# Kernel tuning notes

Measured on AMD Instinct MI355X. Metric: run time of the kernel, lower is better.

Reference implementation:

```python
import jax, jax.numpy as jnp
import numpy as np

STRIDE = 16
RATIOS = (0.5, 1.0, 2.0)
SCALES = (8, 16, 32)
NMS_THRESH = 0.7
NUM_PRE = 12000
NUM_POST = 2000
MIN_SIZE = 16.0


def _all_anchors(feat_h, feat_w):
    # base anchors centered at (stride/2, stride/2), (y1, x1, y2, x2)
    base = []
    for r in RATIOS:
        for s in SCALES:
            h = STRIDE * s * np.sqrt(r)
            w = STRIDE * s * np.sqrt(1.0 / r)
            c = STRIDE / 2.0
            base.append([c - h / 2.0, c - w / 2.0, c + h / 2.0, c + w / 2.0])
    base = np.asarray(base, np.float32)  # (A, 4)
    ys = np.arange(feat_h, dtype=np.float32) * STRIDE
    xs = np.arange(feat_w, dtype=np.float32) * STRIDE
    shift = np.stack(np.meshgrid(ys, xs, indexing='ij'), axis=-1)  # (H, W, 2) = (y, x)
    shift4 = np.concatenate([shift, shift], axis=-1)  # (H, W, 4)
    anchors = shift4[:, :, None, :] + base[None, None, :, :]  # (H, W, A, 4)
    return jnp.asarray(anchors.reshape(-1, 4))


def _conv(x, w, b, padding):
    y = jax.lax.conv_general_dilated(x, w, (1, 1), padding,
                                     dimension_numbers=('NCHW', 'OIHW', 'NCHW'))
    return y + b[None, :, None, None]


def _create_rpn_proposals(locs, scores, anchors, img_h, img_w):
    # box deparameterize (y1,x1,y2,x2 anchors; dy,dx,dh,dw locs)
    ha = anchors[:, 2] - anchors[:, 0]
    wa = anchors[:, 3] - anchors[:, 1]
    cya = anchors[:, 0] + 0.5 * ha
    cxa = anchors[:, 1] + 0.5 * wa
    cy = locs[:, 0] * ha + cya
    cx = locs[:, 1] * wa + cxa
    h = ha * jnp.exp(locs[:, 2])
    w = wa * jnp.exp(locs[:, 3])
    boxes = jnp.stack([cy - 0.5 * h, cx - 0.5 * w, cy + 0.5 * h, cx + 0.5 * w], axis=1)

    order = jnp.argsort(-scores)[:NUM_PRE]
    boxes = boxes[order]
    s = scores[order]

    lim = jnp.array([img_h, img_w, img_h, img_w], dtype=boxes.dtype)
    boxes = jnp.clip(boxes, 0.0, lim)
    valid = ((boxes[:, 2] - boxes[:, 0]) >= MIN_SIZE) & ((boxes[:, 3] - boxes[:, 1]) >= MIN_SIZE)

    areas = (boxes[:, 2] - boxes[:, 0]) * (boxes[:, 3] - boxes[:, 1])
    n = boxes.shape[0]
    idx = jnp.arange(n)

    def body(i, suppressed):
        bi = boxes[i]
        yy1 = jnp.maximum(bi[0], boxes[:, 0])
        xx1 = jnp.maximum(bi[1], boxes[:, 1])
        yy2 = jnp.minimum(bi[2], boxes[:, 2])
        xx2 = jnp.minimum(bi[3], boxes[:, 3])
        inter = jnp.maximum(yy2 - yy1, 0.0) * jnp.maximum(xx2 - xx1, 0.0)
        iou = inter / (areas[i] + areas - inter + 1e-10)
        new_sup = suppressed | ((iou > NMS_THRESH) & (idx > i))
        return jnp.where(suppressed[i], suppressed, new_sup)

    suppressed = jax.lax.fori_loop(0, n, body, ~valid)
    keep = (~suppressed) & valid
    rank = jnp.cumsum(keep) - 1
    tgt = jnp.where(keep & (rank < NUM_POST), rank, NUM_POST)  # overflow slot
    out = jnp.zeros((NUM_POST + 1, 4), boxes.dtype).at[tgt].set(boxes)[:NUM_POST]
    return out  # (2000, 4), zero-padded if fewer kept


def setup_inputs() -> dict:
    key = jax.random.key(0)
    ks = jax.random.split(key, 7)
    in_c, out_c, A = 1024, 512, 9
    x = jax.random.normal(ks[0], (1, in_c, 64, 64), dtype=jnp.float32)
    conv_w = jax.random.normal(ks[1], (out_c, in_c, 3, 3), jnp.float32) * 0.01
    conv_b = jnp.zeros((out_c,), jnp.float32)
    score_w = jax.random.normal(ks[2], (A * 2, out_c, 1, 1), jnp.float32) * 0.01
    score_b = jnp.zeros((A * 2,), jnp.float32)
    loc_w = jax.random.normal(ks[3], (A * 4, out_c, 1, 1), jnp.float32) * 0.01
    loc_b = jnp.zeros((A * 4,), jnp.float32)
    return {"x": x, "conv_w": conv_w, "conv_b": conv_b,
            "score_w": score_w, "score_b": score_b,
            "loc_w": loc_w, "loc_b": loc_b,
            "img_h": 1024, "img_w": 1024}


def reference(x, conv_w, conv_b, score_w, score_b, loc_w, loc_b, img_h, img_w):
    _, _, fh, fw = x.shape
    anchors = _all_anchors(fh, fw)  # (fh*fw*A, 4)
    h = jax.nn.leaky_relu(_conv(x, conv_w, conv_b, 'SAME'), 0.01)
    rpn_locs = _conv(h, loc_w, loc_b, 'VALID').transpose(0, 2, 3, 1).reshape(-1, 4)
    rpn_scores = _conv(h, score_w, score_b, 'VALID').transpose(0, 2, 3, 1).reshape(-1, 2)
    fg = jax.nn.softmax(rpn_scores, axis=1)[:, 1]
    rois = _create_rpn_proposals(jax.lax.stop_gradient(rpn_locs),
                                 jax.lax.stop_gradient(fg),
                                 anchors, img_h, img_w)
    return rpn_locs, rpn_scores, rois, anchors
```

## Files before the change

### kernel.cpp

```cpp
#include <hip/hip_runtime.h>
#include <cstdint>
#include <cstddef>
#include <math.h>

#define NANCH    36864
#define NPRE     12000
#define NPRE_PAD 12032
#define NW       188
#define SORT_N   16384
#define NPOST    2000

typedef double d4_t __attribute__((ext_vector_type(4)));

__device__ __forceinline__ int tribase(int ci) { return ci * NW - (ci * (ci - 1)) / 2; }

typedef __attribute__((address_space(1))) const void* as1cv_t;
typedef __attribute__((address_space(3))) void* as3v_t;
__device__ __forceinline__ void gload_lds16(const float* g, float* l)
{
    __builtin_amdgcn_global_load_lds((as1cv_t)g, (as3v_t)l, 16, 0, 0);
}

__global__ __launch_bounds__(256, 2)
void k_conv_mfma(const float* __restrict__ xg, const float* __restrict__ wg_,
                 const float* __restrict__ bg, float* __restrict__ hg)
{
    __shared__ __align__(16) float wlds[2][4608];
    __shared__ __align__(16) float xlds[2][1632];
    const int tid = threadIdx.x;
    const int oct = blockIdx.x & 7;
    const int y   = blockIdx.x >> 3;
    const int oc0 = oct << 6;
    const int l   = tid & 63;
    const int wv  = tid >> 6;
    const int g   = l >> 4;
    const int li  = l & 15;
    const int wm  = wv >> 1;
    const int wn  = wv & 1;

    int pr[4], qc[4];
    int aG = g;
    {
        d4_t Pz = {0., 0., 0., 0.}, Qz = {0., 0., 0., 0.}, Tz = {0., 0., 0., 0.};
        Pz = __builtin_amdgcn_mfma_f64_16x16x4f64((double)li, 1.0, Pz, 0, 0, 0);
        Qz = __builtin_amdgcn_mfma_f64_16x16x4f64(1.0, (double)li, Qz, 0, 0, 0);
        Tz = __builtin_amdgcn_mfma_f64_16x16x4f64((double)g, (double)(1 << (2 * g)),
                                                  Tz, 0, 0, 0);
        bool ok = true;
        const int tval = (int)Tz[0];
        if ((int)Tz[1] != tval || (int)Tz[2] != tval || (int)Tz[3] != tval) ok = false;
        int seen = 0;
#pragma unroll
        for (int j = 0; j < 4; ++j) {
            int d = (tval >> (2 * j)) & 3;
            seen |= 1 << d;
            if (d == g) aG = j;
        }
        if (seen != 15) ok = false;
#pragma unroll
        for (int r = 0; r < 4; ++r) {
            int pv = (int)Pz[r], qv = (int)Qz[r];
            if ((pv & 3) || (qv & 3)) ok = false;
            pr[r] = pv >> 2; qc[r] = qv >> 2;
            if (pr[r] > 15 || qc[r] > 15) ok = false;
        }
        if (!ok) {
#pragma unroll
            for (int r = 0; r < 4; ++r) { pr[r] = 4 * g + r; qc[r] = li; }
            aG = g;
        }
    }

    d4_t acc00 = {0., 0., 0., 0.}, acc01 = {0., 0., 0., 0.};
    d4_t acc10 = {0., 0., 0., 0.}, acc11 = {0., 0., 0., 0.};

    int xoff[7], loff[7];
#pragma unroll
    for (int t = 0; t < 7; ++t) {
        int f = tid + 256 * t;
        if (f < 1584) {
            int ic = f / 198; int r = f - ic * 198; int sr = r / 66; int gc = r - sr * 66;
            loff[t] = (ic * 3 + sr) * 68 + gc;
            int gy = y + sr - 1, gx = gc - 1;
            xoff[t] = (gy >= 0 && gy < 64 && gx >= 0 && gx < 64)
                      ? (ic * 4096 + gy * 64 + gx) : -1;
        } else { loff[t] = -1; xoff[t] = -1; }
    }

    const float* wsrc0 = wg_ + (size_t)(oc0 + l) * 9216;
    const int abase = wm * 32 + li;
    const int bbase = (wn * 32 + li) * 4 + g;
    float xr[7];

    {
#pragma unroll
        for (int i = 0; i < 5; ++i) {
            int slot = wv + 4 * i;
            if (slot < 18) gload_lds16(wsrc0 + 4 * slot, &wlds[0][slot * 256]);
        }
#pragma unroll
        for (int t = 0; t < 7; ++t) xr[t] = (xoff[t] >= 0) ? xg[xoff[t]] : 0.f;
#pragma unroll
        for (int t = 0; t < 7; ++t)
            if (loff[t] >= 0) xlds[0][loff[t]] = xr[t];
        const float* xp = xg + 32768;
#pragma unroll
        for (int t = 0; t < 7; ++t) xr[t] = (xoff[t] >= 0) ? xp[xoff[t]] : 0.f;
        asm volatile("s_waitcnt lgkmcnt(0)" ::: "memory");
        asm volatile("s_waitcnt vmcnt(0)" ::: "memory");
        __builtin_amdgcn_sched_barrier(0);
        __builtin_amdgcn_s_barrier();
        __builtin_amdgcn_sched_barrier(0);
    }

    int cur = 0;
#pragma unroll 1
    for (int cc = 0; cc < 128; ++cc) {
        if (cc < 127) {
            const float* wsrc = wsrc0 + (cc + 1) * 72;
            float* wdst = &wlds[cur ^ 1][0];
#pragma unroll
            for (int i = 0; i < 5; ++i) {
                int slot = wv + 4 * i;
                if (slot < 18) gload_lds16(wsrc + 4 * slot, wdst + slot * 256);
            }
            __builtin_amdgcn_sched_barrier(0);
            float* xdst = &xlds[cur ^ 1][0];
#pragma unroll
            for (int t = 0; t < 7; ++t)
                if (loff[t] >= 0) xdst[loff[t]] = xr[t];
            __builtin_amdgcn_sched_barrier(0);
            {
                int nc = (cc + 2 < 128) ? (cc + 2) : 127;
                const float* xp = xg + (size_t)nc * 32768;
#pragma unroll
                for (int t = 0; t < 7; ++t) xr[t] = (xoff[t] >= 0) ? xp[xoff[t]] : 0.f;
            }
            __builtin_amdgcn_sched_barrier(0);
            asm volatile("s_waitcnt lgkmcnt(0)" ::: "memory");
            asm volatile("s_waitcnt vmcnt(11)" ::: "memory");
        } else {
            asm volatile("s_waitcnt lgkmcnt(0)" ::: "memory");
            asm volatile("s_waitcnt vmcnt(0)" ::: "memory");
        }
        __builtin_amdgcn_sched_barrier(0);
        __builtin_amdgcn_s_barrier();
        __builtin_amdgcn_sched_barrier(0);

        const float* wb = &wlds[cur][0];
        const float* xb = &xlds[cur][0];
        __builtin_amdgcn_s_setprio(1);
#pragma unroll
        for (int s = 0; s < 18; ++s) {
            int k   = 4 * s + aG;
            int icL = k / 9; int tap = k - 9 * icL;
            int ky  = tap / 3; int kx = tap - 3 * ky;
            int ax  = (icL * 3 + ky) * 68 + kx + abase;
            double a0 = (double)xb[ax];
            double a1 = (double)xb[ax + 16];
            double b0 = (double)wb[bbase + s * 256];
            double b1 = (double)wb[bbase + s * 256 + 64];
            acc00 = __builtin_amdgcn_mfma_f64_16x16x4f64(a0, b0, acc00, 0, 0, 0);
            acc01 = __builtin_amdgcn_mfma_f64_16x16x4f64(a0, b1, acc01, 0, 0, 0);
            acc10 = __builtin_amdgcn_mfma_f64_16x16x4f64(a1, b0, acc10, 0, 0, 0);
            acc11 = __builtin_amdgcn_mfma_f64_16x16x4f64(a1, b1, acc11, 0, 0, 0);
        }
        __builtin_amdgcn_s_setprio(0);
        __builtin_amdgcn_sched_barrier(0);
        asm volatile("s_waitcnt lgkmcnt(0)" ::: "memory");
        __builtin_amdgcn_s_barrier();
        __builtin_amdgcn_sched_barrier(0);
        cur ^= 1;
    }

    __syncthreads();
    float* olds = &wlds[0][0];
    {
#pragma unroll
        for (int r = 0; r < 4; ++r) {
            const int oca = wn * 32 + qc[r];
            const int ocb = oca + 16;
            const double ba = (double)bg[oc0 + oca];
            const double bb = (double)bg[oc0 + ocb];
            const int pxa = wm * 32 + pr[r];
            const int pxb = pxa + 16;
            double t00 = acc00[r] + ba;
            double t01 = acc01[r] + bb;
            double t10 = acc10[r] + ba;
            double t11 = acc11[r] + bb;
            olds[oca * 68 + pxa] = (float)((t00 >= 0.0) ? t00 : 0.01 * t00);
            olds[ocb * 68 + pxa] = (float)((t01 >= 0.0) ? t01 : 0.01 * t01);
            olds[oca * 68 + pxb] = (float)((t10 >= 0.0) ? t10 : 0.01 * t10);
            olds[ocb * 68 + pxb] = (float)((t11 >= 0.0) ? t11 : 0.01 * t11);
        }
    }
    __syncthreads();
    {
        const int oc = tid >> 2, q = tid & 3;
        float* dst = hg + (size_t)(oc0 + oc) * 4096 + y * 64 + q * 16;
        const float* src = &olds[oc * 68 + q * 16];
#pragma unroll
        for (int j = 0; j < 4; ++j)
            *(float4*)(dst + 4 * j) = *(const float4*)(src + 4 * j);
    }
}

__global__ __launch_bounds__(256, 1)
void k_heads(const float* __restrict__ hg, const float* __restrict__ loc_w,
             const float* __restrict__ loc_b, const float* __restrict__ score_w,
             const float* __restrict__ score_b, const int* __restrict__ imh,
             const int* __restrict__ imw, float* __restrict__ out,
             float* __restrict__ boxes_all, unsigned long long* __restrict__ keys64)
{
    __shared__ float  hch[64 * 64];
    __shared__ float  wch[54 * 64];
    __shared__ float  ol[54 * 64];
    __shared__ double sld[18 * 64];
    const int y = blockIdx.x, tid = threadIdx.x;
    const int px = tid & 63, cg = tid >> 6;
    double acc[14];
#pragma unroll
    for (int u = 0; u < 14; ++u) acc[u] = 0.0;
    for (int cc = 0; cc < 8; ++cc) {
        __syncthreads();
#pragma unroll
        for (int t = 0; t < 16; ++t) {
            int f = tid + 256 * t;
            hch[f] = hg[(size_t)(cc * 64 + (f >> 6)) * 4096 + y * 64 + (f & 63)];
        }
#pragma unroll
        for (int t = 0; t < 14; ++t) {
            int f = tid + 256 * t;
            if (f < 54 * 64) {
                int ch = f >> 6, c = f & 63;
                wch[f] = (ch < 36) ? loc_w[ch * 512 + cc * 64 + c]
                                   : score_w[(ch - 36) * 512 + cc * 64 + c];
            }
        }
        __syncthreads();
        for (int c = 0; c < 64; ++c) {
            double hvd = (double)hch[c * 64 + px];
#pragma unroll
            for (int u = 0; u < 14; ++u) {
                int ch = cg + 4 * u;
                if (ch < 54) acc[u] = fma((double)wch[ch * 64 + c], hvd, acc[u]);
            }
        }
    }
    __syncthreads();
#pragma unroll
    for (int u = 0; u < 14; ++u) {
        int ch = cg + 4 * u;
        if (ch < 54) {
            double s = acc[u] + (double)((ch < 36) ? loc_b[ch] : score_b[ch - 36]);
            ol[ch * 64 + px] = (float)s;
            if (ch >= 36) sld[(ch - 36) * 64 + px] = s;
        }
    }
    __syncthreads();
    for (int f = tid; f < 64 * 36; f += 256) {
        int p = f / 36, ch = f - 36 * p;
        out[(size_t)(y * 64 + p) * 36 + ch] = ol[ch * 64 + p];
    }
    for (int f = tid; f < 64 * 18; f += 256) {
        int p = f / 18, ch = f - 18 * p;
        out[147456 + (size_t)(y * 64 + p) * 18 + ch] = ol[(36 + ch) * 64 + p];
    }
    const float fy = (float)(*imh), fx = (float)(*imw);
    float* anch = out + 229184;
    for (int t2 = tid; t2 < 576; t2 += 256) {
        int p = t2 / 9, a = t2 - 9 * p;
        int pg = y * 64 + p;
        int ar = a / 3, as = a - 3 * ar;
        double rr = (ar == 0) ? 0.5 : ((ar == 1) ? 1.0 : 2.0);
        double ss = (as == 0) ? 8.0 : ((as == 1) ? 16.0 : 32.0);
        double hh = 16.0 * ss * sqrt(rr), wwd = 16.0 * ss * sqrt(1.0 / rr);
        float by1 = (float)(8.0 - hh * 0.5), bx1 = (float)(8.0 - wwd * 0.5);
        float by2 = (float)(8.0 + hh * 0.5), bx2 = (float)(8.0 + wwd * 0.5);
        float sy = (float)(y * 16), sx = (float)(p * 16);
        float a0 = sy + by1, a1 = sx + bx1, a2 = sy + by2, a3 = sx + bx2;
        int base = (pg * 9 + a) * 4;
        anch[base + 0] = a0; anch[base + 1] = a1; anch[base + 2] = a2; anch[base + 3] = a3;
        double d = sld[(a * 2 + 1) * 64 + p] - sld[(a * 2) * 64 + p];
        long long bits = __double_as_longlong(d);
        unsigned long long u64 =
            (unsigned long long)(bits ^ ((bits >> 63) | (long long)0x8000000000000000LL));
        unsigned long long v = ~u64;
        keys64[pg * 9 + a] = (v & 0xFFFFFFFFFFFF0000ULL) | (unsigned long long)(pg * 9 + a);
        float dy = ol[(a * 4 + 0) * 64 + p], dxv = ol[(a * 4 + 1) * 64 + p];
        float dh = ol[(a * 4 + 2) * 64 + p], dwv = ol[(a * 4 + 3) * 64 + p];
        float hA = a2 - a0, wA = a3 - a1;
        float cya = a0 + 0.5f * hA, cxa = a1 + 0.5f * wA;
        float cy = dy * hA + cya, cx = dxv * wA + cxa;
        float hb = hA * expf(dh), wb = wA * expf(dwv);
        float b0 = fminf(fmaxf(cy - 0.5f * hb, 0.f), fy);
        float b1 = fminf(fmaxf(cx - 0.5f * wb, 0.f), fx);
        float b2 = fminf(fmaxf(cy + 0.5f * hb, 0.f), fy);
        float b3 = fminf(fmaxf(cx + 0.5f * wb, 0.f), fx);
        boxes_all[base + 0] = b0; boxes_all[base + 1] = b1;
        boxes_all[base + 2] = b2; boxes_all[base + 3] = b3;
    }
}

__global__ __launch_bounds__(1024, 1)
void k_select(const unsigned long long* __restrict__ keys64,
              const float* __restrict__ boxes_all,
              unsigned long long* __restrict__ sortbuf, float* __restrict__ sbox,
              float* __restrict__ areas, unsigned long long* __restrict__ suppr)
{
    __shared__ unsigned int hist[256];
    __shared__ unsigned int sh_below, sh_prefix, sh_nsel;
    __shared__ unsigned long long tile[4096];
    const int tid = threadIdx.x;
    if (tid == 0) { sh_below = 0; sh_prefix = 0; sh_nsel = 0; }
    __syncthreads();
    for (int p = 3; p >= 0; --p) {
        if (tid < 256) hist[tid] = 0;
        __syncthreads();
        unsigned int pref = sh_prefix;
        int shift = p * 8;
        for (int i = tid; i < NANCH; i += 1024) {
            unsigned int k = (unsigned int)(keys64[i] >> 32);
            bool match = (p == 3) || ((k >> (shift + 8)) == pref);
            if (match) atomicAdd(&hist[(k >> shift) & 255u], 1u);
        }
        __syncthreads();
        if (tid == 0) {
            unsigned int below = sh_below, cacc = 0;
            int b = 0;
            for (; b < 256; ++b) {
                if (below + cacc + hist[b] >= NPRE) break;
                cacc += hist[b];
            }
            if (b > 255) b = 255;
            sh_below = below + cacc;
            sh_prefix = (pref << 8) | (unsigned int)b;
        }
        __syncthreads();
    }
    const unsigned int P = sh_prefix;
    for (int i = tid; i < NANCH; i += 1024) {
        unsigned long long k = keys64[i];
        if ((unsigned int)(k >> 32) <= P) {
            unsigned int pos = atomicAdd(&sh_nsel, 1u);
            if (pos < SORT_N) sortbuf[pos] = k;
        }
    }
    __syncthreads();
    unsigned int nsel = sh_nsel; if (nsel > SORT_N) nsel = SORT_N;
    for (unsigned int i = nsel + tid; i < SORT_N; i += 1024) sortbuf[i] = ~0ULL;
    __syncthreads();
    for (int T = 0; T < 4; ++T) {
        for (int t = tid; t < 4096; t += 1024) tile[t] = sortbuf[T * 4096 + t];
        __syncthreads();
        for (int k2 = 2; k2 <= 4096; k2 <<= 1) {
            for (int j = k2 >> 1; j > 0; j >>= 1) {
                for (int t = tid; t < 2048; t += 1024) {
                    int i = ((t & ~(j - 1)) << 1) | (t & (j - 1));
                    int ip = i | j;
                    bool up = (((T * 4096 + i) & k2) == 0);
                    unsigned long long A = tile[i], B = tile[ip];
                    if ((A > B) == up) { tile[i] = B; tile[ip] = A; }
                }
                __syncthreads();
            }
        }
        for (int t = tid; t < 4096; t += 1024) sortbuf[T * 4096 + t] = tile[t];
        __syncthreads();
    }
    auto gstage = [&](int k2, int j) {
        for (int t = tid; t < 8192; t += 1024) {
            int i = ((t & ~(j - 1)) << 1) | (t & (j - 1));
            int ip = i | j;
            bool up = ((i & k2) == 0);
            unsigned long long A = sortbuf[i], B = sortbuf[ip];
            if ((A > B) == up) { sortbuf[i] = B; sortbuf[ip] = A; }
        }
        __syncthreads();
    };
    auto ltail = [&](int k2) {
        for (int T = 0; T < 4; ++T) {
            for (int t = tid; t < 4096; t += 1024) tile[t] = sortbuf[T * 4096 + t];
            __syncthreads();
            for (int j = 2048; j > 0; j >>= 1) {
                for (int t = tid; t < 2048; t += 1024) {
                    int i = ((t & ~(j - 1)) << 1) | (t & (j - 1));
                    int ip = i | j;
                    bool up = (((T * 4096 + i) & k2) == 0);
                    unsigned long long A = tile[i], B = tile[ip];
                    if ((A > B) == up) { tile[i] = B; tile[ip] = A; }
                }
                __syncthreads();
            }
            for (int t = tid; t < 4096; t += 1024) sortbuf[T * 4096 + t] = tile[t];
            __syncthreads();
        }
    };
    gstage(8192, 4096);  ltail(8192);
    gstage(16384, 8192); gstage(16384, 4096); ltail(16384);

    if (tid < NW) suppr[tid] = (tid == NW - 1) ? 0xFFFFFFFF00000000ULL : 0ULL;
    __syncthreads();
    for (int r = tid; r < NPRE_PAD; r += 1024) {
        float b0 = 0, b1 = 0, b2 = 0, b3 = 0;
        if (r < NPRE) {
            unsigned int idx = (unsigned int)(sortbuf[r] & 0xFFFFULL);
            const float* bp = boxes_all + (size_t)idx * 4;
            b0 = bp[0]; b1 = bp[1]; b2 = bp[2]; b3 = bp[3];
        }
        sbox[r * 4 + 0] = b0; sbox[r * 4 + 1] = b1;
        sbox[r * 4 + 2] = b2; sbox[r * 4 + 3] = b3;
        areas[r] = (b2 - b0) * (b3 - b1);
        if (r < NPRE) {
            bool valid = ((b2 - b0) >= 16.0f) && ((b3 - b1) >= 16.0f);
            if (!valid) atomicOr(&suppr[r >> 6], 1ULL << (r & 63));
        }
    }
}

__global__ __launch_bounds__(256, 1)
void k_mask(const float* __restrict__ sbox, const float* __restrict__ areas,
            unsigned long long* __restrict__ mask)
{
    const int cj = blockIdx.x, q = blockIdx.y;
    __shared__ float4 bx[64];
    __shared__ float aj[64];
    const int t = threadIdx.x;
    const int j0 = cj * 64;
    if (t < 64) { bx[t] = ((const float4*)sbox)[j0 + t]; aj[t] = areas[j0 + t]; }
    __syncthreads();
    const int c0 = ((cj + 1) * q) >> 2, c1 = ((cj + 1) * (q + 1)) >> 2;
    for (int i0 = c0 * 64; i0 < c1 * 64; i0 += 256) {
        int i = i0 + t;
        if (i < c1 * 64) {
            const float4 p = ((const float4*)sbox)[i];
            const float ai = areas[i];
            unsigned long long w = 0;
            for (int jj = 0; jj < 64; ++jj) {
                float4 qb = bx[jj];
                float yy1 = fmaxf(p.x, qb.x), xx1 = fmaxf(p.y, qb.y);
                float yy2 = fminf(p.z, qb.z), xx2 = fminf(p.w, qb.w);
                float inter = fmaxf(yy2 - yy1, 0.f) * fmaxf(xx2 - xx1, 0.f);
                float iou = inter / (ai + aj[jj] - inter + 1e-10f);
                w |= ((unsigned long long)((iou > 0.7f) && (j0 + jj > i))) << jj;
            }
            int ci = i >> 6;
            mask[(size_t)(tribase(ci) + (cj - ci)) * 64 + (i & 63)] = w;
        }
    }
}

__global__ __launch_bounds__(256, 1)
void k_scan(const unsigned long long* __restrict__ mask,
            const unsigned long long* __restrict__ suppr,
            const float* __restrict__ sbox, float* __restrict__ rois)
{
    __shared__ unsigned long long rvs[NW];
    __shared__ unsigned long long curw;
    __shared__ unsigned long long keptw[NW];
    __shared__ int totkept, brk;
    __shared__ int pref[NW + 1];
    const int tid = threadIdx.x;
    if (tid < NW) { rvs[tid] = suppr[tid]; keptw[tid] = 0ULL; }
    if (tid == 0) { totkept = 0; brk = 0; }
    __syncthreads();
    for (int c = 0; c < NW; ++c) {
        if (tid < 64) {
            unsigned long long diag = mask[(size_t)tribase(c) * 64 + tid];
            unsigned long long w = rvs[c];
            for (int b = 0; b < 64; ++b) {
                unsigned long long db = __shfl(diag, b, 64);
                if (!((w >> b) & 1ULL)) w |= db;
            }
            if (tid == 0) {
                curw = w;
                keptw[c] = ~w;
                totkept += __popcll(~w);
                if (totkept >= NPOST) brk = 1;
            }
        }
        __syncthreads();
        if (brk) break;
        unsigned long long kw = ~curw;
        if (kw && tid > c && tid < NW) {
            const unsigned long long* mrow = mask + (size_t)(tribase(c) + (tid - c)) * 64;
            unsigned long long a0 = 0, a1 = 0, a2 = 0, a3 = 0;
            while (kw) {
                int b0 = -1, b1 = -1, b2 = -1, b3 = -1;
                b0 = (int)__builtin_ctzll(kw); kw &= kw - 1;
                if (kw) { b1 = (int)__builtin_ctzll(kw); kw &= kw - 1; }
                if (kw) { b2 = (int)__builtin_ctzll(kw); kw &= kw - 1; }
                if (kw) { b3 = (int)__builtin_ctzll(kw); kw &= kw - 1; }
                unsigned long long m0 = mrow[b0];
                unsigned long long m1 = (b1 >= 0) ? mrow[b1] : 0ULL;
                unsigned long long m2 = (b2 >= 0) ? mrow[b2] : 0ULL;
                unsigned long long m3 = (b3 >= 0) ? mrow[b3] : 0ULL;
                a0 |= m0; a1 |= m1; a2 |= m2; a3 |= m3;
            }
            rvs[tid] |= a0 | a1 | a2 | a3;
        }
        __syncthreads();
    }
    __syncthreads();
    if (tid == 0) {
        int s = 0;
        for (int c = 0; c < NW; ++c) { pref[c] = s; s += __popcll(keptw[c]); }
        pref[NW] = s;
    }
    __syncthreads();
    int total = pref[NW]; if (total > NPOST) total = NPOST;
    for (int r = total * 4 + tid; r < NPOST * 4; r += 256) rois[r] = 0.f;
    if (tid < NW) {
        unsigned long long kw = keptw[tid];
        int r = pref[tid];
        for (int b = 0; b < 64; ++b) {
            if ((kw >> b) & 1ULL) {
                if (r < NPOST) {
                    const float* bp = sbox + (size_t)(tid * 64 + b) * 4;
                    rois[r * 4 + 0] = bp[0]; rois[r * 4 + 1] = bp[1];
                    rois[r * 4 + 2] = bp[2]; rois[r * 4 + 3] = bp[3];
                }
                ++r;
            }
        }
    }
}

extern "C" void kernel_launch(void* const* d_in, const int* in_sizes, int n_in,
                              void* d_out, int out_size, void* d_ws, size_t ws_size,
                              hipStream_t stream)
{
    const float* x       = (const float*)d_in[0];
    const float* conv_w  = (const float*)d_in[1];
    const float* conv_b  = (const float*)d_in[2];
    const float* score_w = (const float*)d_in[3];
    const float* score_b = (const float*)d_in[4];
    const float* loc_w   = (const float*)d_in[5];
    const float* loc_b   = (const float*)d_in[6];
    const int*   imh     = (const int*)d_in[7];
    const int*   imw     = (const int*)d_in[8];
    float* out = (float*)d_out;
    char* ws = (char*)d_ws;
    float* h                    = (float*)(ws);
    float* boxes_all            = (float*)(ws + 8388608);
    unsigned long long* keys64  = (unsigned long long*)(ws + 8978432);
    float* sbox                 = (float*)(ws + 9273344);
    float* areas                = (float*)(ws + 9465856);
    unsigned long long* suppr   = (unsigned long long*)(ws + 9513984);
    unsigned long long* sortbuf = (unsigned long long*)(ws + 9515520);
    unsigned long long* mask    = (unsigned long long*)(ws + 9646592);

    k_conv_mfma<<<512, 256, 0, stream>>>(x, conv_w, conv_b, h);
    k_heads <<<64, 256, 0, stream>>>(h, loc_w, loc_b, score_w, score_b, imh, imw,
                                     out, boxes_all, keys64);
    k_select<<<1, 1024, 0, stream>>>(keys64, boxes_all, sortbuf, sbox, areas, suppr);
    k_mask  <<<dim3(188, 4), 256, 0, stream>>>(sbox, areas, mask);
    k_scan  <<<1, 256, 0, stream>>>(mask, suppr, sbox, out + 221184);
}
```

Before: 1.724 ms.

## Triple-buffer conv LDS to drop a barrier, prefetch NMS diagonal words

```diff
diff --git a/kernel.cpp b/kernel.cpp
--- a/kernel.cpp
+++ b/kernel.cpp
@@ -25,8 +25,8 @@
 void k_conv_mfma(const float* __restrict__ xg, const float* __restrict__ wg_,
                  const float* __restrict__ bg, float* __restrict__ hg)
 {
-    __shared__ __align__(16) float wlds[2][4608];
-    __shared__ __align__(16) float xlds[2][1632];
+    __shared__ __align__(16) float wlds[3][4608];
+    __shared__ __align__(16) float xlds[3][1632];
     const int tid = threadIdx.x;
     const int oct = blockIdx.x & 7;
     const int y   = blockIdx.x >> 3;
@@ -37,6 +37,7 @@
     const int li  = l & 15;
     const int wm  = wv >> 1;
     const int wn  = wv & 1;
+    const int slot5 = 16 + (wv & 1);
 
     int pr[4], qc[4];
     int aG = g;
@@ -86,6 +87,9 @@
                       ? (ic * 4096 + gy * 64 + gx) : -1;
         } else { loff[t] = -1; xoff[t] = -1; }
     }
+    int xoffL[7];
+#pragma unroll
+    for (int t = 0; t < 7; ++t) xoffL[t] = (xoff[t] >= 0) ? xoff[t] : 0;
 
     const float* wsrc0 = wg_ + (size_t)(oc0 + l) * 9216;
     const int abase = wm * 32 + li;
@@ -94,18 +98,17 @@
 
     {
 #pragma unroll
-        for (int i = 0; i < 5; ++i) {
-            int slot = wv + 4 * i;
-            if (slot < 18) gload_lds16(wsrc0 + 4 * slot, &wlds[0][slot * 256]);
-        }
-#pragma unroll
-        for (int t = 0; t < 7; ++t) xr[t] = (xoff[t] >= 0) ? xg[xoff[t]] : 0.f;
+        for (int i = 0; i < 4; ++i)
+            gload_lds16(wsrc0 + 4 * (wv + 4 * i), &wlds[0][(wv + 4 * i) * 256]);
+        gload_lds16(wsrc0 + 4 * slot5, &wlds[0][slot5 * 256]);
+#pragma unroll
+        for (int t = 0; t < 7; ++t) xr[t] = xg[xoffL[t]];
 #pragma unroll
         for (int t = 0; t < 7; ++t)
-            if (loff[t] >= 0) xlds[0][loff[t]] = xr[t];
+            if (loff[t] >= 0) xlds[0][loff[t]] = (xoff[t] >= 0) ? xr[t] : 0.f;
         const float* xp = xg + 32768;
 #pragma unroll
-        for (int t = 0; t < 7; ++t) xr[t] = (xoff[t] >= 0) ? xp[xoff[t]] : 0.f;
+        for (int t = 0; t < 7; ++t) xr[t] = xp[xoffL[t]];
         asm volatile("s_waitcnt lgkmcnt(0)" ::: "memory");
         asm volatile("s_waitcnt vmcnt(0)" ::: "memory");
         __builtin_amdgcn_sched_barrier(0);
@@ -116,29 +119,29 @@
     int cur = 0;
 #pragma unroll 1
     for (int cc = 0; cc < 128; ++cc) {
+        int nxt = cur + 1; if (nxt == 3) nxt = 0;
         if (cc < 127) {
             const float* wsrc = wsrc0 + (cc + 1) * 72;
-            float* wdst = &wlds[cur ^ 1][0];
-#pragma unroll
-            for (int i = 0; i < 5; ++i) {
-                int slot = wv + 4 * i;
-                if (slot < 18) gload_lds16(wsrc + 4 * slot, wdst + slot * 256);
-            }
+            float* wdst = &wlds[nxt][0];
+#pragma unroll
+            for (int i = 0; i < 4; ++i)
+                gload_lds16(wsrc + 4 * (wv + 4 * i), wdst + (wv + 4 * i) * 256);
+            gload_lds16(wsrc + 4 * slot5, wdst + slot5 * 256);
             __builtin_amdgcn_sched_barrier(0);
-            float* xdst = &xlds[cur ^ 1][0];
+            float* xdst = &xlds[nxt][0];
 #pragma unroll
             for (int t = 0; t < 7; ++t)
-                if (loff[t] >= 0) xdst[loff[t]] = xr[t];
+                if (loff[t] >= 0) xdst[loff[t]] = (xoff[t] >= 0) ? xr[t] : 0.f;
             __builtin_amdgcn_sched_barrier(0);
             {
                 int nc = (cc + 2 < 128) ? (cc + 2) : 127;
                 const float* xp = xg + (size_t)nc * 32768;
 #pragma unroll
-                for (int t = 0; t < 7; ++t) xr[t] = (xoff[t] >= 0) ? xp[xoff[t]] : 0.f;
+                for (int t = 0; t < 7; ++t) xr[t] = xp[xoffL[t]];
             }
             __builtin_amdgcn_sched_barrier(0);
             asm volatile("s_waitcnt lgkmcnt(0)" ::: "memory");
-            asm volatile("s_waitcnt vmcnt(11)" ::: "memory");
+            asm volatile("s_waitcnt vmcnt(12)" ::: "memory");
         } else {
             asm volatile("s_waitcnt lgkmcnt(0)" ::: "memory");
             asm volatile("s_waitcnt vmcnt(0)" ::: "memory");
@@ -166,11 +169,7 @@
             acc11 = __builtin_amdgcn_mfma_f64_16x16x4f64(a1, b1, acc11, 0, 0, 0);
         }
         __builtin_amdgcn_s_setprio(0);
-        __builtin_amdgcn_sched_barrier(0);
-        asm volatile("s_waitcnt lgkmcnt(0)" ::: "memory");
-        __builtin_amdgcn_s_barrier();
-        __builtin_amdgcn_sched_barrier(0);
-        cur ^= 1;
+        cur = nxt;
     }
 
     __syncthreads();
@@ -458,15 +457,20 @@
     __shared__ unsigned long long rvs[NW];
     __shared__ unsigned long long curw;
     __shared__ unsigned long long keptw[NW];
+    __shared__ unsigned long long diagbuf[2][64];
     __shared__ int totkept, brk;
     __shared__ int pref[NW + 1];
     const int tid = threadIdx.x;
     if (tid < NW) { rvs[tid] = suppr[tid]; keptw[tid] = 0ULL; }
     if (tid == 0) { totkept = 0; brk = 0; }
+    if (tid < 64) diagbuf[0][tid] = mask[tid];
     __syncthreads();
     for (int c = 0; c < NW; ++c) {
+        unsigned long long pf = 0;
+        const bool isPf = (tid >= 64 && tid < 128 && c + 1 < NW);
+        if (isPf) pf = mask[((size_t)tribase(c + 1)) * 64 + (tid - 64)];
         if (tid < 64) {
-            unsigned long long diag = mask[(size_t)tribase(c) * 64 + tid];
+            unsigned long long diag = diagbuf[c & 1][tid];
             unsigned long long w = rvs[c];
             for (int b = 0; b < 64; ++b) {
                 unsigned long long db = __shfl(diag, b, 64);
@@ -484,21 +488,23 @@
         unsigned long long kw = ~curw;
         if (kw && tid > c && tid < NW) {
             const unsigned long long* mrow = mask + (size_t)(tribase(c) + (tid - c)) * 64;
-            unsigned long long a0 = 0, a1 = 0, a2 = 0, a3 = 0;
+            unsigned long long acc = 0;
             while (kw) {
-                int b0 = -1, b1 = -1, b2 = -1, b3 = -1;
-                b0 = (int)__builtin_ctzll(kw); kw &= kw - 1;
-                if (kw) { b1 = (int)__builtin_ctzll(kw); kw &= kw - 1; }
-                if (kw) { b2 = (int)__builtin_ctzll(kw); kw &= kw - 1; }
-                if (kw) { b3 = (int)__builtin_ctzll(kw); kw &= kw - 1; }
-                unsigned long long m0 = mrow[b0];
-                unsigned long long m1 = (b1 >= 0) ? mrow[b1] : 0ULL;
-                unsigned long long m2 = (b2 >= 0) ? mrow[b2] : 0ULL;
-                unsigned long long m3 = (b3 >= 0) ? mrow[b3] : 0ULL;
-                a0 |= m0; a1 |= m1; a2 |= m2; a3 |= m3;
-            }
-            rvs[tid] |= a0 | a1 | a2 | a3;
-        }
+                unsigned long long m0 = 0, m1 = 0, m2 = 0, m3 = 0,
+                                   m4 = 0, m5 = 0, m6 = 0, m7 = 0;
+                int b = (int)__builtin_ctzll(kw); m0 = mrow[b]; kw &= kw - 1;
+                if (kw) { b = (int)__builtin_ctzll(kw); m1 = mrow[b]; kw &= kw - 1; }
+                if (kw) { b = (int)__builtin_ctzll(kw); m2 = mrow[b]; kw &= kw - 1; }
+                if (kw) { b = (int)__builtin_ctzll(kw); m3 = mrow[b]; kw &= kw - 1; }
+                if (kw) { b = (int)__builtin_ctzll(kw); m4 = mrow[b]; kw &= kw - 1; }
+                if (kw) { b = (int)__builtin_ctzll(kw); m5 = mrow[b]; kw &= kw - 1; }
+                if (kw) { b = (int)__builtin_ctzll(kw); m6 = mrow[b]; kw &= kw - 1; }
+                if (kw) { b = (int)__builtin_ctzll(kw); m7 = mrow[b]; kw &= kw - 1; }
+                acc |= ((m0 | m1) | (m2 | m3)) | ((m4 | m5) | (m6 | m7));
+            }
+            rvs[tid] |= acc;
+        }
+        if (isPf) diagbuf[(c + 1) & 1][tid - 64] = pf;
         __syncthreads();
     }
     __syncthreads();
```

New measurement: 1.706 ms. No clear change (-1.1%).
